# Kernel optimization log

Measured on AMD Instinct MI355X. Metric: run time of the kernel, lower is better.

Reference implementation:

```python
import jax, jax.numpy as jnp
import numpy as np

B, L, C, S, W, R = 2, 32, 32, 64, 64, 32
MH = 32  # forcing MLP hidden


def _conv3d(x, w, b, pad_hw):
    # x: [B, Cin, L, S, W], w: [Cout, Cin, 1, kh, kw]
    y = jax.lax.conv_general_dilated(
        x, w, window_strides=(1, 1, 1),
        padding=[(0, 0), (pad_hw, pad_hw), (pad_hw, pad_hw)],
        dimension_numbers=('NCDHW', 'OIDHW', 'NCDHW'))
    return y + b[None, :, None, None, None]


def _forward(x, listT, params_log_base, dispersion_mod, fm_W1, fm_b1, fm_W2, fm_b2,
             forcing_scale, U_re, U_im, V_re, V_im, pW_re, pW_im, pb_re, pb_im,
             convr_w, convr_b, convi_w, convi_b, projc_w, projc_b, ln_w, ln_b):
    b, l, c, s, w = x.shape
    r = U_re.shape[-1]
    pad = s // 4
    dt = listT.reshape(b, l, 1, 1, 1)

    # FFT with mirror padding along S
    xp = jnp.pad(x, ((0, 0), (0, 0), (0, 0), (pad, pad), (0, 0)), mode='reflect')
    h = jnp.fft.fft2(xp.astype(jnp.complex64), axes=(-2, -1), norm='ortho')

    # complex channel projection
    proj_W = pW_re + 1j * pW_im
    h = jnp.einsum('blcsw,cd->bldsw', h, proj_W)
    h = h + (pb_re + 1j * pb_im)[None, None, :, None, None]

    # back to spatial, crop pad, re-FFT
    hs = jnp.fft.ifft2(h, axes=(-2, -1), norm='ortho')[..., pad:-pad, :]
    h = jnp.fft.fft2(hs, axes=(-2, -1), norm='ortho')

    U = U_re + 1j * U_im          # [C, S, R]
    V = V_re + 1j * V_im          # [C, W, R]
    # zq[b,l,c,r,q] = sum_{s,w} h * conj(U)[c,s,r] * V[c,w,q]
    zq = jnp.einsum('blcsw,csr,cwq->blcrq', h, jnp.conj(U), V)

    nu_base = jnp.exp(params_log_base[0] + dispersion_mod[0]).reshape(1, 1, c, r, 1)
    th_base = jnp.exp(params_log_base[1] + dispersion_mod[1]).reshape(1, 1, c, r, 1)

    # forcing modulation
    ctx = x.mean(axis=(-2, -1))                       # [B, L, C]
    inp = jnp.concatenate([ctx, dt.reshape(b, l, 1)], axis=-1)
    mid = jnp.tanh(inp @ fm_W1 + fm_b1)
    mod = (mid @ fm_W2 + fm_b2).reshape(b, l, c, r, 2)
    dnu = (forcing_scale * jnp.tanh(mod[..., 0]))[..., None]
    dth = (forcing_scale * jnp.tanh(mod[..., 1]))[..., None]

    nu_t = jnp.maximum(nu_base * dt + dnu, 1e-6)       # [B, L, C, R, 1]
    th_t = th_base * dt + dth
    lamb = jnp.exp(jax.lax.complex(-nu_t, th_t))       # complex [B, L, C, R, 1]

    gamma = jnp.sqrt(jnp.maximum(1.0 - jnp.exp(-2.0 * nu_t), 1e-12))
    x_in = zq * gamma.astype(zq.dtype)                 # [B, L, C, R, R]

    # parallel linear-recurrence scan: z_t = lamb_t * z_{t-1} + x_t
    def comb(a, bb):
        a1, x1 = a
        a2, x2 = bb
        return a1 * a2, a2 * x1 + x2
    _, z_out = jax.lax.associative_scan(comb, (lamb, x_in), axis=1)

    # reconstruct spectral field and inverse FFT
    h_rec = jnp.einsum('blcrq,cwq,csr->blcsw', z_out, jnp.conj(V), U)
    h_sp = jnp.fft.ifft2(h_rec, axes=(-2, -1), norm='ortho')

    xr = jnp.transpose(h_sp.real, (0, 2, 1, 3, 4))     # [B, C, L, S, W]
    xi = jnp.transpose(h_sp.imag, (0, 2, 1, 3, 4))
    hr = _conv3d(xr, convr_w, convr_b, 1)
    hi = _conv3d(xi, convi_w, convi_b, 1)
    hf = _conv3d(jnp.concatenate([hr, hi], axis=1), projc_w, projc_b, 0)
    hf = jnp.transpose(hf, (0, 2, 1, 3, 4))            # [B, L, C, S, W]

    # LayerNorm over [S, W]
    mu = hf.mean(axis=(-2, -1), keepdims=True)
    var = hf.var(axis=(-2, -1), keepdims=True)
    hf = (hf - mu) / jnp.sqrt(var + 1e-5) * ln_w + ln_b

    return x + hf


def setup_inputs() -> dict:
    key = jax.random.key(0)
    ks = jax.random.split(key, 20)
    f32 = jnp.float32
    x = jax.random.normal(ks[0], (B, L, C, S, W), dtype=f32)
    listT = jax.random.uniform(ks[1], (B, L), dtype=f32, minval=0.5, maxval=1.5)

    r_min, r_max = 0.8, 0.99
    u1 = jax.random.uniform(ks[2], (C, R), dtype=f32)
    u2 = jax.random.uniform(ks[3], (C, R), dtype=f32)
    nu_log = jnp.log(-0.5 * jnp.log(u1 * (r_max ** 2 - r_min ** 2) + r_min ** 2))
    theta_log = jnp.log(u2 * (2.0 * np.pi))
    params_log_base = jnp.stack([nu_log, theta_log], axis=0)
    dispersion_mod = jnp.zeros((2, C, R), dtype=f32)

    fm_W1 = jax.random.normal(ks[4], (C + 1, MH), dtype=f32) / np.sqrt(C + 1)
    fm_b1 = jnp.zeros((MH,), dtype=f32)
    fm_W2 = jax.random.normal(ks[5], (MH, C * R * 2), dtype=f32) / np.sqrt(MH)
    fm_b2 = jnp.zeros((C * R * 2,), dtype=f32)
    forcing_scale = jnp.float32(0.1)

    cplx_scale = 1.0 / np.sqrt(2.0)
    U_re = jax.random.normal(ks[6], (C, S, R), dtype=f32) * cplx_scale / np.sqrt(S)
    U_im = jax.random.normal(ks[7], (C, S, R), dtype=f32) * cplx_scale / np.sqrt(S)
    V_re = jax.random.normal(ks[8], (C, W, R), dtype=f32) * cplx_scale / np.sqrt(W)
    V_im = jax.random.normal(ks[9], (C, W, R), dtype=f32) * cplx_scale / np.sqrt(W)
    pW_re = jax.random.normal(ks[10], (C, C), dtype=f32) * cplx_scale / np.sqrt(C)
    pW_im = jax.random.normal(ks[11], (C, C), dtype=f32) * cplx_scale / np.sqrt(C)
    pb_re = jnp.zeros((C,), dtype=f32)
    pb_im = jnp.zeros((C,), dtype=f32)

    convr_w = jax.random.normal(ks[12], (C, C, 1, 3, 3), dtype=f32) * (1.0 / np.sqrt(C * 9))
    convr_b = jnp.zeros((C,), dtype=f32)
    convi_w = jax.random.normal(ks[13], (C, C, 1, 3, 3), dtype=f32) * (1.0 / np.sqrt(C * 9))
    convi_b = jnp.zeros((C,), dtype=f32)
    projc_w = jax.random.normal(ks[14], (C, 2 * C, 1, 1, 1), dtype=f32) * (1.0 / np.sqrt(2 * C))
    projc_b = jnp.zeros((C,), dtype=f32)

    ln_w = jnp.ones((S, W), dtype=f32)
    ln_b = jnp.zeros((S, W), dtype=f32)

    return dict(x=x, listT=listT, params_log_base=params_log_base,
                dispersion_mod=dispersion_mod, fm_W1=fm_W1, fm_b1=fm_b1,
                fm_W2=fm_W2, fm_b2=fm_b2, forcing_scale=forcing_scale,
                U_re=U_re, U_im=U_im, V_re=V_re, V_im=V_im,
                pW_re=pW_re, pW_im=pW_im, pb_re=pb_re, pb_im=pb_im,
                convr_w=convr_w, convr_b=convr_b, convi_w=convi_w, convi_b=convi_b,
                projc_w=projc_w, projc_b=projc_b, ln_w=ln_w, ln_b=ln_b)


def reference(x, listT, params_log_base, dispersion_mod, fm_W1, fm_b1, fm_W2, fm_b2,
              forcing_scale, U_re, U_im, V_re, V_im, pW_re, pW_im, pb_re, pb_im,
              convr_w, convr_b, convi_w, convi_b, projc_w, projc_b, ln_w, ln_b):
    return _forward(x, listT, params_log_base, dispersion_mod, fm_W1, fm_b1, fm_W2,
                    fm_b2, forcing_scale, U_re, U_im, V_re, V_im, pW_re, pW_im,
                    pb_re, pb_im, convr_w, convr_b, convi_w, convi_b, projc_w,
                    projc_b, ln_w, ln_b)
```

## Files before the change

### kernel.cpp

```cpp
#include <hip/hip_runtime.h>


typedef __attribute__((ext_vector_type(8))) short short8;
typedef __attribute__((ext_vector_type(4))) float floatx4;

__device__ __forceinline__ unsigned pack_bf16(float re, float im) {
  unsigned a = __float_as_uint(re), b = __float_as_uint(im);
  a = (a + 0x7FFFu + ((a >> 16) & 1u)) >> 16;
  b = (b + 0x7FFFu + ((b >> 16) & 1u)) >> 16;
  return a | (b << 16);
}
__device__ __forceinline__ unsigned short bf16r(float v) {
  unsigned a = __float_as_uint(v);
  return (unsigned short)((a + 0x7FFFu + ((a >> 16) & 1u)) >> 16);
}

__global__ __launch_bounds__(256) void k_prep(
    const float* __restrict__ U_re, const float* __restrict__ U_im,
    const float* __restrict__ V_re, const float* __restrict__ V_im,
    const float* __restrict__ projc_w,
    const float* __restrict__ convr_w, const float* __restrict__ convi_w,
    const float* __restrict__ x,
    unsigned* __restrict__ zqA, unsigned* __restrict__ recA,
    unsigned* __restrict__ recB, unsigned* __restrict__ Wtb,
    float* __restrict__ ctx) {
  const int bid = blockIdx.x;
  const int tid = threadIdx.x;
  if (bid < 2048) {
    __shared__ float2 tw[64];
    if (tid < 64) {
      float sa, ca;
      sincosf((float)tid * 0.09817477042468103f, &sa, &ca);
      tw[tid] = make_float2(ca, sa);
    }
    __syncthreads();
    int gid = bid * 256 + tid;
    const float *Ar, *Ai;
    int knum, mode, variant;
    bool plus;
    unsigned* dst;
    int didx;
    if (gid < 262144) {
      int c = gid >> 13, mat = (gid >> 11) & 3, m = (gid >> 6) & 31,
          kw = gid & 63;
      knum = kw; mode = m;
      if (mat < 2) { Ar = V_re + c * 2048; Ai = V_im + c * 2048; plus = false; }
      else         { Ar = U_re + c * 2048; Ai = U_im + c * 2048; plus = true; }
      variant = mat; dst = zqA; didx = gid;
    } else {
      int rid = gid - 262144;
      int c = rid >> 13, sub = rid & 8191;
      int which = sub >> 11, mm = (sub >> 5) & 63, k2 = sub & 31;
      knum = mm; mode = k2;
      if (which < 2) {
        Ar = U_re + c * 2048; Ai = U_im + c * 2048; plus = true;
        variant = 4 + which; dst = recA;
        didx = ((c * 2 + which) * 64 + mm) * 32 + k2;
      } else {
        Ar = V_re + c * 2048; Ai = V_im + c * 2048; plus = false;
        variant = 4 + which; dst = recB;
        didx = ((c * 2 + which - 2) * 64 + mm) * 32 + k2;
      }
    }
    float sr = 0.f, si = 0.f;
    for (int n = 0; n < 64; ++n) {
      float2 w = tw[(knum * n) & 63];
      float ar = Ar[n * 32 + mode], ai = Ai[n * 32 + mode];
      if (plus) { sr += ar * w.x - ai * w.y; si += ar * w.y + ai * w.x; }
      else      { sr += ar * w.x + ai * w.y; si += ai * w.x - ar * w.y; }
    }
    sr *= 0.125f; si *= 0.125f;
    unsigned pv;
    switch (variant) {
      case 0: pv = pack_bf16(sr, -si); break;
      case 1: pv = pack_bf16(si, sr); break;
      case 2: pv = pack_bf16(sr, si); break;
      case 3: pv = pack_bf16(-si, sr); break;
      case 4: pv = pack_bf16(sr, -si); break;
      case 5: pv = pack_bf16(si, sr); break;
      case 6: pv = pack_bf16(sr, si); break;
      default: pv = pack_bf16(-si, sr); break;
    }
    dst[didx] = pv;
  } else if (bid < 2084) {
    int gid = (bid - 2048) * 256 + tid;
    if (gid < 9216) {
      int co = gid / 288;
      int r2 = gid - co * 288;
      int tap = r2 >> 5, ci = r2 & 31;
      float sr = 0.f, si = 0.f;
      for (int m = 0; m < 32; ++m) {
        sr += projc_w[co * 64 + m]      * convr_w[(m * 32 + ci) * 9 + tap];
        si += projc_w[co * 64 + 32 + m] * convi_w[(m * 32 + ci) * 9 + tap];
      }
      Wtb[gid] = pack_bf16(sr, si);
    }
  } else {
    int blc = bid - 2084;
    const float* p = x + (size_t)blc * 4096;
    float s = 0.f;
    for (int i = tid; i < 4096; i += 256) s += p[i];
    for (int o = 32; o > 0; o >>= 1) s += __shfl_down(s, o, 64);
    __shared__ float wsum[4];
    if ((tid & 63) == 0) wsum[tid >> 6] = s;
    __syncthreads();
    if (tid == 0)
      ctx[blc] = (wsum[0] + wsum[1] + wsum[2] + wsum[3]) * (1.f / 4096.f);
  }
}

__global__ __launch_bounds__(256) void k_mix_mlp(
    const float* __restrict__ x, const float* __restrict__ pWr,
    const float* __restrict__ pWi, unsigned* __restrict__ hs,
    const float* __restrict__ ctx, const float* __restrict__ listT,
    const float* __restrict__ plb, const float* __restrict__ dmod,
    const float* __restrict__ W1, const float* __restrict__ b1,
    const float* __restrict__ W2, const float* __restrict__ b2,
    const float* __restrict__ fscale,
    float2* __restrict__ lam, float* __restrict__ gam) {
  __shared__ unsigned xb_s[512 * 20];
  __shared__ float mid_s[32];
  const int tid = threadIdx.x;
  if (blockIdx.x < 512) {
    const int bl = blockIdx.x >> 3;
    const int pxbase = (blockIdx.x & 7) * 512;
    const float* xb = x + (size_t)bl * 131072 + pxbase;
#pragma unroll
    for (int t = 0; t < 8; ++t) {
      int i = t * 256 + tid;
      int c2 = i & 15, g4 = i >> 4;
      float4 a = *(const float4*)(xb + (2 * c2) * 4096 + g4 * 4);
      float4 b = *(const float4*)(xb + (2 * c2 + 1) * 4096 + g4 * 4);
#pragma unroll
      for (int j = 0; j < 4; ++j) {
        int px = g4 * 4 + j;
        xb_s[px * 20 + (((c2 >> 2) ^ (px & 3)) << 2) + (c2 & 3)] =
            pack_bf16(((const float*)&a)[j], ((const float*)&b)[j]);
      }
    }
    const int lane = tid & 63, wv = tid >> 6;
    const int qd = lane >> 4, ln = lane & 15;
    short8 arL, aiL, arH, aiH;
#pragma unroll
    for (int j = 0; j < 8; ++j) {
      int ci = qd * 8 + j;
      ((short*)&arL)[j] = (short)bf16r(pWr[ci * 32 + ln]);
      ((short*)&aiL)[j] = (short)bf16r(pWi[ci * 32 + ln]);
      ((short*)&arH)[j] = (short)bf16r(pWr[ci * 32 + 16 + ln]);
      ((short*)&aiH)[j] = (short)bf16r(pWi[ci * 32 + 16 + ln]);
    }
    __syncthreads();
#pragma unroll
    for (int pt = 0; pt < 8; ++pt) {
      int pxt = wv * 8 + pt;
      int pxl = pxt * 16 + ln;
      short8 bfr =
          *(const short8*)&xb_s[pxl * 20 + ((qd ^ (pxl & 3)) << 2)];
      floatx4 dRL = {0.f, 0.f, 0.f, 0.f}, dIL = {0.f, 0.f, 0.f, 0.f};
      floatx4 dRH = {0.f, 0.f, 0.f, 0.f}, dIH = {0.f, 0.f, 0.f, 0.f};
      dRL = __builtin_amdgcn_mfma_f32_16x16x32_bf16(arL, bfr, dRL, 0, 0, 0);
      dIL = __builtin_amdgcn_mfma_f32_16x16x32_bf16(aiL, bfr, dIL, 0, 0, 0);
      dRH = __builtin_amdgcn_mfma_f32_16x16x32_bf16(arH, bfr, dRH, 0, 0, 0);
      dIH = __builtin_amdgcn_mfma_f32_16x16x32_bf16(aiH, bfr, dIH, 0, 0, 0);
      unsigned* ho = hs + (size_t)bl * 131072 + pxbase + pxt * 16 + ln;
#pragma unroll
      for (int j = 0; j < 4; ++j) {
        ho[(qd * 4 + j) * 4096] = pack_bf16(dRL[j], dIL[j]);
        ho[(16 + qd * 4 + j) * 4096] = pack_bf16(dRH[j], dIH[j]);
      }
    }
  } else {
    int bl = blockIdx.x - 512;
    float dt = listT[bl];
    if (tid < 32) {
      float a = b1[tid];
      for (int j = 0; j < 32; ++j) a += ctx[bl * 32 + j] * W1[j * 32 + tid];
      a += dt * W1[1024 + tid];
      mid_s[tid] = tanhf(a);
    }
    __syncthreads();
    float fs = fscale[0];
#pragma unroll
    for (int u = 0; u < 4; ++u) {
      int cr = u * 256 + tid;
      int col = cr * 2;
      float m0 = b2[col], m1 = b2[col + 1];
      for (int h = 0; h < 32; ++h) {
        float mh = mid_s[h];
        float2 w2 = *(const float2*)&W2[h * 2048 + col];
        m0 += mh * w2.x;
        m1 += mh * w2.y;
      }
      float dnu = fs * tanhf(m0);
      float dth = fs * tanhf(m1);
      float nub = expf(plb[cr] + dmod[cr]);
      float thb = expf(plb[1024 + cr] + dmod[1024 + cr]);
      float nut = fmaxf(nub * dt + dnu, 1e-6f);
      float tht = thb * dt + dth;
      float e = expf(-nut);
      float sa, ca;
      sincosf(tht, &sa, &ca);
      float g = sqrtf(fmaxf(1.f - expf(-2.f * nut), 1e-12f));
      int o = bl * 1024 + cr;
      lam[o] = make_float2(e * ca, e * sa);
      gam[o] = g;
    }
  }
}

__global__ __launch_bounds__(256) void k_zq(const unsigned* __restrict__ hs,
                                            const short* __restrict__ zqA,
                                            float2* __restrict__ zq) {
  __shared__ unsigned HsB[4096];
  __shared__ unsigned T2[2048];
  const int blc = blockIdx.x;
  const int c = blc & 31;
  const int tid = threadIdx.x;
  const int lane = tid & 63, wv = tid >> 6;
  const int qd = lane >> 4, ln = lane & 15;
  const int mt = wv >> 1, nth = wv & 1;
  {
    const uint4* hp = (const uint4*)(hs + (size_t)blc * 4096);
#pragma unroll
    for (int it = 0; it < 4; ++it) {
      int i4 = tid + it * 256;
      uint4 v = hp[i4];
      int s = i4 >> 4, w4 = i4 & 15;
      *(uint4*)&HsB[s * 64 + ((w4 ^ (s & 15)) << 2)] = v;
    }
  }
  const short* zA = zqA + (size_t)c * 4 * 32 * 128;
  short8 a1[4], a2[4], a3[4], a4[4];
#pragma unroll
  for (int t = 0; t < 4; ++t) {
    int row = mt * 16 + ln;
    a1[t] = *(const short8*)(zA + (0 * 32 + row) * 128 + t * 32 + qd * 8);
    a2[t] = *(const short8*)(zA + (1 * 32 + row) * 128 + t * 32 + qd * 8);
    a3[t] = *(const short8*)(zA + (2 * 32 + row) * 128 + t * 32 + qd * 8);
    a4[t] = *(const short8*)(zA + (3 * 32 + row) * 128 + t * 32 + qd * 8);
  }
  __syncthreads();
#pragma unroll
  for (int nti = 0; nti < 2; ++nti) {
    int nt = nth * 2 + nti;
    int n = nt * 16 + ln;
    floatx4 accr = {0.f, 0.f, 0.f, 0.f}, acci = {0.f, 0.f, 0.f, 0.f};
#pragma unroll
    for (int t = 0; t < 4; ++t) {
      short8 b = *(const short8*)&HsB[n * 64 + (((4 * t + qd) ^ (n & 15)) << 2)];
      accr = __builtin_amdgcn_mfma_f32_16x16x32_bf16(a1[t], b, accr, 0, 0, 0);
      acci = __builtin_amdgcn_mfma_f32_16x16x32_bf16(a2[t], b, acci, 0, 0, 0);
    }
#pragma unroll
    for (int j = 0; j < 4; ++j) {
      int q = mt * 16 + qd * 4 + j;
      int s = n;
      T2[q * 64 + (((s >> 2) ^ (q & 15)) << 2) + (s & 3)] = pack_bf16(accr[j], acci[j]);
    }
  }
  __syncthreads();
  {
    const int mt2 = wv >> 1, nt2 = wv & 1;
    int n = nt2 * 16 + ln;
    floatx4 zr = {0.f, 0.f, 0.f, 0.f}, zi = {0.f, 0.f, 0.f, 0.f};
#pragma unroll
    for (int t = 0; t < 4; ++t) {
      short8 b = *(const short8*)&T2[n * 64 + (((4 * t + qd) ^ (n & 15)) << 2)];
      zr = __builtin_amdgcn_mfma_f32_16x16x32_bf16(a3[t], b, zr, 0, 0, 0);
      zi = __builtin_amdgcn_mfma_f32_16x16x32_bf16(a4[t], b, zi, 0, 0, 0);
    }
    float2* zo = zq + (size_t)blc * 1024;
#pragma unroll
    for (int j = 0; j < 4; ++j) {
      int r = mt2 * 16 + qd * 4 + j;
      zo[r * 32 + n] = make_float2(zr[j], zi[j]);
    }
  }
}

__global__ __launch_bounds__(256) void k_scan(const float2* __restrict__ lam,
                                              const float* __restrict__ gam,
                                              const float2* zin,
                                              float2* zout) {
  const int b = blockIdx.x >> 5, c = blockIdx.x & 31;
  const int tid = threadIdx.x;
  float2 st[4] = {{0.f, 0.f}, {0.f, 0.f}, {0.f, 0.f}, {0.f, 0.f}};
  float2 v[4], lmv[4];
  float gv[4];
  {
    size_t zb = ((size_t)(b * 32) * 32 + c) * 1024;
    int pb = (b * 32) * 1024 + c * 32;
#pragma unroll
    for (int j = 0; j < 4; ++j) {
      int rq = tid + 256 * j;
      v[j] = zin[zb + rq];
      lmv[j] = lam[pb + (rq >> 5)];
      gv[j] = gam[pb + (rq >> 5)];
    }
  }
  for (int t = 0; t < 32; ++t) {
    float2 nv[4], nlm[4];
    float ng[4];
    if (t < 31) {
      size_t zb = ((size_t)(b * 32 + t + 1) * 32 + c) * 1024;
      int pb = (b * 32 + t + 1) * 1024 + c * 32;
#pragma unroll
      for (int j = 0; j < 4; ++j) {
        int rq = tid + 256 * j;
        nv[j] = zin[zb + rq];
        nlm[j] = lam[pb + (rq >> 5)];
        ng[j] = gam[pb + (rq >> 5)];
      }
    }
    size_t zb = ((size_t)(b * 32 + t) * 32 + c) * 1024;
#pragma unroll
    for (int j = 0; j < 4; ++j) {
      float nr = lmv[j].x * st[j].x - lmv[j].y * st[j].y + gv[j] * v[j].x;
      float ni = lmv[j].x * st[j].y + lmv[j].y * st[j].x + gv[j] * v[j].y;
      st[j] = make_float2(nr, ni);
      zout[zb + tid + 256 * j] = st[j];
    }
#pragma unroll
    for (int j = 0; j < 4; ++j) { v[j] = nv[j]; lmv[j] = nlm[j]; gv[j] = ng[j]; }
  }
}

__global__ __launch_bounds__(256) void k_rec(const float2* __restrict__ zs,
                                             const short* __restrict__ recA,
                                             const short* __restrict__ recB,
                                             unsigned* __restrict__ hsp) {
  __shared__ unsigned zB[1024];
  __shared__ unsigned P[2048];
  const int blc = blockIdx.x;
  const int c = blc & 31;
  const int tid = threadIdx.x;
  const int lane = tid & 63, wv = tid >> 6;
  const int qd = lane >> 4, ln = lane & 15;
  {
    const float2* zp = zs + (size_t)blc * 1024;
#pragma unroll
    for (int it = 0; it < 4; ++it) {
      int i = tid + it * 256;
      float2 v = zp[i];
      int r = i >> 5, q = i & 31;
      zB[q * 32 + (((r >> 2) ^ (q & 7)) << 2) + (r & 3)] = pack_bf16(v.x, v.y);
    }
  }
  const short* rA = recA + (size_t)c * 2 * 64 * 64;
  short8 a5[2], a6[2];
#pragma unroll
  for (int t = 0; t < 2; ++t) {
    int row = wv * 16 + ln;
    a5[t] = *(const short8*)(rA + (0 * 64 + row) * 64 + t * 32 + qd * 8);
    a6[t] = *(const short8*)(rA + (1 * 64 + row) * 64 + t * 32 + qd * 8);
  }
  __syncthreads();
#pragma unroll
  for (int nt = 0; nt < 2; ++nt) {
    int n = nt * 16 + ln;
    floatx4 pr = {0.f, 0.f, 0.f, 0.f}, pi = {0.f, 0.f, 0.f, 0.f};
#pragma unroll
    for (int t = 0; t < 2; ++t) {
      short8 b = *(const short8*)&zB[n * 32 + (((4 * t + qd) ^ (n & 7)) << 2)];
      pr = __builtin_amdgcn_mfma_f32_16x16x32_bf16(a5[t], b, pr, 0, 0, 0);
      pi = __builtin_amdgcn_mfma_f32_16x16x32_bf16(a6[t], b, pi, 0, 0, 0);
    }
#pragma unroll
    for (int j = 0; j < 4; ++j) {
      int s = wv * 16 + qd * 4 + j;
      int q = n;
      P[s * 32 + (((q >> 2) ^ (s & 7)) << 2) + (q & 3)] = pack_bf16(pr[j], pi[j]);
    }
  }
  __syncthreads();
  const short* rB = recB + (size_t)c * 2 * 64 * 64;
  short8 pa[2];
#pragma unroll
  for (int t = 0; t < 2; ++t) {
    int row = wv * 16 + ln;
    pa[t] = *(const short8*)&P[row * 32 + (((4 * t + qd) ^ (row & 7)) << 2)];
  }
#pragma unroll
  for (int nt = 0; nt < 4; ++nt) {
    int n = nt * 16 + ln;
    floatx4 hr = {0.f, 0.f, 0.f, 0.f}, hi = {0.f, 0.f, 0.f, 0.f};
#pragma unroll
    for (int t = 0; t < 2; ++t) {
      short8 b5 = *(const short8*)(rB + (0 * 64 + n) * 64 + t * 32 + qd * 8);
      short8 b6 = *(const short8*)(rB + (1 * 64 + n) * 64 + t * 32 + qd * 8);
      hr = __builtin_amdgcn_mfma_f32_16x16x32_bf16(pa[t], b5, hr, 0, 0, 0);
      hi = __builtin_amdgcn_mfma_f32_16x16x32_bf16(pa[t], b6, hi, 0, 0, 0);
    }
    unsigned* ho = hsp + (size_t)blc * 4096;
#pragma unroll
    for (int j = 0; j < 4; ++j) {
      int s = wv * 16 + qd * 4 + j;
      ho[s * 64 + n] = pack_bf16(hr[j], hi[j]);
    }
  }
}

__global__ __launch_bounds__(256, 2) void k_conv(
    const unsigned* __restrict__ hsp, const short* __restrict__ Wtb,
    unsigned short* __restrict__ convout, float2* __restrict__ stats) {
  __shared__ unsigned lds_in[6 * 66 * 32];
  const int bl = blockIdx.x >> 4;
  const int slab = blockIdx.x & 15;
  const int y0 = slab * 4;
  const int tid = threadIdx.x;
  for (int i = tid; i < 384; i += 256) {
    int ci = i & 31, j = i >> 5;
    int yi = j >> 1, xi = (j & 1) ? 65 : 0;
    int slot = (ci >> 2) ^ (xi & 7);
    lds_in[(yi * 66 + xi) * 32 + slot * 4 + (ci & 3)] = 0u;
  }
#pragma unroll
  for (int t = 0; t < 12; ++t) {
    int i = t * 256 + tid;
    int ci = i & 31;
    int j = i >> 5;
    int yi = j >> 4, x4 = j & 15;
    int y = y0 + yi - 1;
    uint4 v = make_uint4(0u, 0u, 0u, 0u);
    if ((unsigned)y < 64u)
      v = *(const uint4*)(hsp + (((size_t)bl * 32 + ci) * 64 + y) * 64 + x4 * 4);
    int xb = 1 + x4 * 4;
#pragma unroll
    for (int jj = 0; jj < 4; ++jj) {
      int xi = xb + jj;
      int slot = (ci >> 2) ^ (xi & 7);
      lds_in[(yi * 66 + xi) * 32 + slot * 4 + (ci & 3)] =
          ((const unsigned*)&v)[jj];
    }
  }
  const int lane = tid & 63;
  const int wv = tid >> 6;
  const int co = lane & 15;
  const int qd = lane >> 4;
  short8 bL[18], bH[18];
  {
    const short* wpL = Wtb + (co * 9) * 64 + qd * 8;
    const short* wpH = Wtb + ((co + 16) * 9) * 64 + qd * 8;
#pragma unroll
    for (int tap = 0; tap < 9; ++tap)
#pragma unroll
      for (int kk = 0; kk < 2; ++kk) {
        bL[tap * 2 + kk] = *(const short8*)(wpL + tap * 64 + kk * 32);
        bH[tap * 2 + kk] = *(const short8*)(wpH + tap * 64 + kk * 32);
      }
  }
  __syncthreads();
  float sL = 0.f, s2L = 0.f, sH = 0.f, s2H = 0.f;
  const int x0 = wv * 16;
  const int xl = lane & 15;
  for (int ry = 0; ry < 4; ++ry) {
    floatx4 aL = {0.f, 0.f, 0.f, 0.f}, aH = {0.f, 0.f, 0.f, 0.f};
#pragma unroll
    for (int tap = 0; tap < 9; ++tap) {
      int dy = tap / 3, dx = tap - dy * 3;
      int yi = ry + dy;
      int xi = x0 + xl + dx;
#pragma unroll
      for (int kk = 0; kk < 2; ++kk) {
        int slot = ((kk << 2) | qd) ^ (xi & 7);
        const short8 a =
            *(const short8*)&lds_in[(yi * 66 + xi) * 32 + slot * 4];
        aL = __builtin_amdgcn_mfma_f32_16x16x32_bf16(a, bL[tap * 2 + kk], aL, 0, 0, 0);
        aH = __builtin_amdgcn_mfma_f32_16x16x32_bf16(a, bH[tap * 2 + kk], aH, 0, 0, 0);
      }
    }
    size_t goL = (((size_t)bl * 32 + co) * 64 + (y0 + ry)) * 64 + x0 + qd * 4;
    size_t goH = goL + (size_t)16 * 4096;
    *(uint2*)(convout + goL) =
        make_uint2(pack_bf16(aL[0], aL[1]), pack_bf16(aL[2], aL[3]));
    *(uint2*)(convout + goH) =
        make_uint2(pack_bf16(aH[0], aH[1]), pack_bf16(aH[2], aH[3]));
#pragma unroll
    for (int j = 0; j < 4; ++j) {
      sL += aL[j]; s2L += aL[j] * aL[j];
      sH += aH[j]; s2H += aH[j] * aH[j];
    }
  }
  sL += __shfl_down(sL, 32, 64);  s2L += __shfl_down(s2L, 32, 64);
  sH += __shfl_down(sH, 32, 64);  s2H += __shfl_down(s2H, 32, 64);
  sL += __shfl_down(sL, 16, 64);  s2L += __shfl_down(s2L, 16, 64);
  sH += __shfl_down(sH, 16, 64);  s2H += __shfl_down(s2H, 16, 64);
  if (lane < 16) {
    stats[((size_t)bl * 32 + lane) * 64 + slab * 4 + wv] = make_float2(sL, s2L);
    stats[((size_t)bl * 32 + 16 + lane) * 64 + slab * 4 + wv] =
        make_float2(sH, s2H);
  }
}

__global__ __launch_bounds__(256) void k_ln(
    const unsigned short* __restrict__ convout,
    const float2* __restrict__ stats, const float* __restrict__ x,
    const float* __restrict__ ln_w, const float* __restrict__ ln_b,
    float* __restrict__ out) {
  const int blc = blockIdx.x;
  const int tid = threadIdx.x;
  __shared__ float sh_mu, sh_rs;
  if (tid < 64) {
    float2 v = stats[(size_t)blc * 64 + tid];
    float s = v.x, s2 = v.y;
#pragma unroll
    for (int o = 32; o > 0; o >>= 1) {
      s += __shfl_down(s, o, 64);
      s2 += __shfl_down(s2, o, 64);
    }
    if (tid == 0) {
      float mu = s * (1.f / 4096.f);
      float var = s2 * (1.f / 4096.f) - mu * mu;
      sh_mu = mu;
      sh_rs = rsqrtf(var + 1e-5f);
    }
  }
  __syncthreads();
  float mu = sh_mu, rs = sh_rs;
  const uint2* cp = (const uint2*)(convout + (size_t)blc * 4096);
  const float4* xp = (const float4*)(x + (size_t)blc * 4096);
  const float4* lwp = (const float4*)ln_w;
  const float4* lbp = (const float4*)ln_b;
  float4* op = (float4*)(out + (size_t)blc * 4096);
#pragma unroll
  for (int k = 0; k < 4; ++k) {
    int i = tid + k * 256;
    uint2 cv = cp[i];
    float4 xv = xp[i], lw = lwp[i], lb = lbp[i];
    float c0 = __uint_as_float(cv.x << 16);
    float c1 = __uint_as_float(cv.x & 0xFFFF0000u);
    float c2 = __uint_as_float(cv.y << 16);
    float c3 = __uint_as_float(cv.y & 0xFFFF0000u);
    float4 o;
    o.x = xv.x + (c0 - mu) * rs * lw.x + lb.x;
    o.y = xv.y + (c1 - mu) * rs * lw.y + lb.y;
    o.z = xv.z + (c2 - mu) * rs * lw.z + lb.z;
    o.w = xv.w + (c3 - mu) * rs * lw.w + lb.w;
    op[i] = o;
  }
}

extern "C" void kernel_launch(void* const* d_in, const int* in_sizes, int n_in,
                              void* d_out, int out_size, void* d_ws,
                              size_t ws_size, hipStream_t stream) {
  const float* x       = (const float*)d_in[0];
  const float* listT   = (const float*)d_in[1];
  const float* plb     = (const float*)d_in[2];
  const float* dmod    = (const float*)d_in[3];
  const float* fm_W1   = (const float*)d_in[4];
  const float* fm_b1   = (const float*)d_in[5];
  const float* fm_W2   = (const float*)d_in[6];
  const float* fm_b2   = (const float*)d_in[7];
  const float* fscale  = (const float*)d_in[8];
  const float* U_re    = (const float*)d_in[9];
  const float* U_im    = (const float*)d_in[10];
  const float* V_re    = (const float*)d_in[11];
  const float* V_im    = (const float*)d_in[12];
  const float* pW_re   = (const float*)d_in[13];
  const float* pW_im   = (const float*)d_in[14];
  const float* convr_w = (const float*)d_in[17];
  const float* convi_w = (const float*)d_in[19];
  const float* projc_w = (const float*)d_in[21];
  const float* ln_w    = (const float*)d_in[23];
  const float* ln_b    = (const float*)d_in[24];
  float* out = (float*)d_out;

  float* wsf = (float*)d_ws;
  unsigned* hs  = (unsigned*)wsf;
  unsigned* hsp = (unsigned*)wsf;
  unsigned* zqAp  = (unsigned*)(wsf + 8388608);
  unsigned* recAp = (unsigned*)(wsf + 8388608 + 262144);
  unsigned* recBp = (unsigned*)(wsf + 8388608 + 393216);
  unsigned short* convout = (unsigned short*)(wsf + 8388608);
  float2*   stats = (float2*)(wsf + 12582912);
  float2*   zq  = (float2*)(wsf + 16777216);
  size_t off = 16777216 + 4194304;
  float2* zs = (float2*)(wsf + off);
  size_t need_with_zs = (size_t)(off + 4194304 + 470016) * 4;
  bool sep = ws_size >= need_with_zs;
  if (sep) off += 4194304; else zs = zq;
  float2*   lam  = (float2*)(wsf + off);
  float*    gam  = wsf + off + 131072;
  float*    ctx  = wsf + off + 458752;
  unsigned* Wtb  = (unsigned*)(wsf + off + 460800);

  k_prep<<<4132, 256, 0, stream>>>(U_re, U_im, V_re, V_im, projc_w,
                                   convr_w, convi_w, x, zqAp, recAp, recBp,
                                   Wtb, ctx);
  k_mix_mlp<<<576, 256, 0, stream>>>(x, pW_re, pW_im, hs, ctx, listT, plb,
                                     dmod, fm_W1, fm_b1, fm_W2, fm_b2,
                                     fscale, lam, gam);
  k_zq<<<2048, 256, 0, stream>>>(hs, (const short*)zqAp, zq);
  k_scan<<<64, 256, 0, stream>>>(lam, gam, zq, zs);
  k_rec<<<2048, 256, 0, stream>>>(zs, (const short*)recAp, (const short*)recBp, hsp);
  k_conv<<<1024, 256, 0, stream>>>(hsp, (const short*)Wtb, convout, stats);
  k_ln<<<2048, 256, 0, stream>>>(convout, stats, x, ln_w, ln_b, out);
}
```

Measured before the change: 258.8 us.

## Fuse channel-mean into mix kernel, move MLP into zq kernel, widen scan grid

Computes the per-(b,l,c) spatial mean inside the channel-mix kernel while x is already being loaded, accumulating it into ctx with atomics. This removes the separate reduction pass over x in the prep kernel, which now only zeroes ctx. The forcing MLP blocks move into the zq kernel as extra blocks so they can read the completed ctx. The scan kernel goes from 64 to 256 blocks with one element per thread, giving more parallelism on a latency-bound sequential loop. The costs are atomic accumulation, whose summation order can vary between runs, and extra shared-memory reservation in the zq blocks.

```diff
diff --git a/kernel.cpp b/kernel.cpp
--- a/kernel.cpp
+++ b/kernel.cpp
@@ -20,7 +20,6 @@
     const float* __restrict__ V_re, const float* __restrict__ V_im,
     const float* __restrict__ projc_w,
     const float* __restrict__ convr_w, const float* __restrict__ convi_w,
-    const float* __restrict__ x,
     unsigned* __restrict__ zqA, unsigned* __restrict__ recA,
     unsigned* __restrict__ recB, unsigned* __restrict__ Wtb,
     float* __restrict__ ctx) {
@@ -96,81 +95,92 @@
       Wtb[gid] = pack_bf16(sr, si);
     }
   } else {
-    int blc = bid - 2084;
-    const float* p = x + (size_t)blc * 4096;
-    float s = 0.f;
-    for (int i = tid; i < 4096; i += 256) s += p[i];
-    for (int o = 32; o > 0; o >>= 1) s += __shfl_down(s, o, 64);
-    __shared__ float wsum[4];
-    if ((tid & 63) == 0) wsum[tid >> 6] = s;
-    __syncthreads();
-    if (tid == 0)
-      ctx[blc] = (wsum[0] + wsum[1] + wsum[2] + wsum[3]) * (1.f / 4096.f);
-  }
-}
-
-__global__ __launch_bounds__(256) void k_mix_mlp(
+    for (int i = tid; i < 2048; i += 256) ctx[i] = 0.f;
+  }
+}
+
+__global__ __launch_bounds__(256) void k_mix(
     const float* __restrict__ x, const float* __restrict__ pWr,
     const float* __restrict__ pWi, unsigned* __restrict__ hs,
+    float* __restrict__ ctx) {
+  __shared__ unsigned xb_s[512 * 20];
+  __shared__ float red[16][16][2];
+  const int tid = threadIdx.x;
+  const int bl = blockIdx.x >> 3;
+  const int pxbase = (blockIdx.x & 7) * 512;
+  const float* xb = x + (size_t)bl * 131072 + pxbase;
+  float csa = 0.f, csb = 0.f;
+#pragma unroll
+  for (int t = 0; t < 8; ++t) {
+    int i = t * 256 + tid;
+    int c2 = i & 15, g4 = i >> 4;
+    float4 a = *(const float4*)(xb + (2 * c2) * 4096 + g4 * 4);
+    float4 b = *(const float4*)(xb + (2 * c2 + 1) * 4096 + g4 * 4);
+    csa += a.x + a.y + a.z + a.w;
+    csb += b.x + b.y + b.z + b.w;
+#pragma unroll
+    for (int j = 0; j < 4; ++j) {
+      int px = g4 * 4 + j;
+      xb_s[px * 20 + (((c2 >> 2) ^ (px & 3)) << 2) + (c2 & 3)] =
+          pack_bf16(((const float*)&a)[j], ((const float*)&b)[j]);
+    }
+  }
+  red[tid & 15][tid >> 4][0] = csa;
+  red[tid & 15][tid >> 4][1] = csb;
+  const int lane = tid & 63, wv = tid >> 6;
+  const int qd = lane >> 4, ln = lane & 15;
+  short8 arL, aiL, arH, aiH;
+#pragma unroll
+  for (int j = 0; j < 8; ++j) {
+    int ci = qd * 8 + j;
+    ((short*)&arL)[j] = (short)bf16r(pWr[ci * 32 + ln]);
+    ((short*)&aiL)[j] = (short)bf16r(pWi[ci * 32 + ln]);
+    ((short*)&arH)[j] = (short)bf16r(pWr[ci * 32 + 16 + ln]);
+    ((short*)&aiH)[j] = (short)bf16r(pWi[ci * 32 + 16 + ln]);
+  }
+  __syncthreads();
+  if (tid < 32) {
+    int c2 = tid >> 1, part = tid & 1;
+    float s = 0.f;
+#pragma unroll
+    for (int w = 0; w < 16; ++w) s += red[c2][w][part];
+    atomicAdd(&ctx[bl * 32 + 2 * c2 + part], s * (1.f / 4096.f));
+  }
+#pragma unroll
+  for (int pt = 0; pt < 8; ++pt) {
+    int pxt = wv * 8 + pt;
+    int pxl = pxt * 16 + ln;
+    short8 bfr = *(const short8*)&xb_s[pxl * 20 + ((qd ^ (pxl & 3)) << 2)];
+    floatx4 dRL = {0.f, 0.f, 0.f, 0.f}, dIL = {0.f, 0.f, 0.f, 0.f};
+    floatx4 dRH = {0.f, 0.f, 0.f, 0.f}, dIH = {0.f, 0.f, 0.f, 0.f};
+    dRL = __builtin_amdgcn_mfma_f32_16x16x32_bf16(arL, bfr, dRL, 0, 0, 0);
+    dIL = __builtin_amdgcn_mfma_f32_16x16x32_bf16(aiL, bfr, dIL, 0, 0, 0);
+    dRH = __builtin_amdgcn_mfma_f32_16x16x32_bf16(arH, bfr, dRH, 0, 0, 0);
+    dIH = __builtin_amdgcn_mfma_f32_16x16x32_bf16(aiH, bfr, dIH, 0, 0, 0);
+    unsigned* ho = hs + (size_t)bl * 131072 + pxbase + pxt * 16 + ln;
+#pragma unroll
+    for (int j = 0; j < 4; ++j) {
+      ho[(qd * 4 + j) * 4096] = pack_bf16(dRL[j], dIL[j]);
+      ho[(16 + qd * 4 + j) * 4096] = pack_bf16(dRH[j], dIH[j]);
+    }
+  }
+}
+
+__global__ __launch_bounds__(256) void k_zq(
+    const unsigned* __restrict__ hs, const short* __restrict__ zqA,
+    float2* __restrict__ zq,
     const float* __restrict__ ctx, const float* __restrict__ listT,
     const float* __restrict__ plb, const float* __restrict__ dmod,
     const float* __restrict__ W1, const float* __restrict__ b1,
     const float* __restrict__ W2, const float* __restrict__ b2,
     const float* __restrict__ fscale,
     float2* __restrict__ lam, float* __restrict__ gam) {
-  __shared__ unsigned xb_s[512 * 20];
+  __shared__ unsigned HsB[4096];
+  __shared__ unsigned T2[2048];
   __shared__ float mid_s[32];
   const int tid = threadIdx.x;
-  if (blockIdx.x < 512) {
-    const int bl = blockIdx.x >> 3;
-    const int pxbase = (blockIdx.x & 7) * 512;
-    const float* xb = x + (size_t)bl * 131072 + pxbase;
-#pragma unroll
-    for (int t = 0; t < 8; ++t) {
-      int i = t * 256 + tid;
-      int c2 = i & 15, g4 = i >> 4;
-      float4 a = *(const float4*)(xb + (2 * c2) * 4096 + g4 * 4);
-      float4 b = *(const float4*)(xb + (2 * c2 + 1) * 4096 + g4 * 4);
-#pragma unroll
-      for (int j = 0; j < 4; ++j) {
-        int px = g4 * 4 + j;
-        xb_s[px * 20 + (((c2 >> 2) ^ (px & 3)) << 2) + (c2 & 3)] =
-            pack_bf16(((const float*)&a)[j], ((const float*)&b)[j]);
-      }
-    }
-    const int lane = tid & 63, wv = tid >> 6;
-    const int qd = lane >> 4, ln = lane & 15;
-    short8 arL, aiL, arH, aiH;
-#pragma unroll
-    for (int j = 0; j < 8; ++j) {
-      int ci = qd * 8 + j;
-      ((short*)&arL)[j] = (short)bf16r(pWr[ci * 32 + ln]);
-      ((short*)&aiL)[j] = (short)bf16r(pWi[ci * 32 + ln]);
-      ((short*)&arH)[j] = (short)bf16r(pWr[ci * 32 + 16 + ln]);
-      ((short*)&aiH)[j] = (short)bf16r(pWi[ci * 32 + 16 + ln]);
-    }
-    __syncthreads();
-#pragma unroll
-    for (int pt = 0; pt < 8; ++pt) {
-      int pxt = wv * 8 + pt;
-      int pxl = pxt * 16 + ln;
-      short8 bfr =
-          *(const short8*)&xb_s[pxl * 20 + ((qd ^ (pxl & 3)) << 2)];
-      floatx4 dRL = {0.f, 0.f, 0.f, 0.f}, dIL = {0.f, 0.f, 0.f, 0.f};
-      floatx4 dRH = {0.f, 0.f, 0.f, 0.f}, dIH = {0.f, 0.f, 0.f, 0.f};
-      dRL = __builtin_amdgcn_mfma_f32_16x16x32_bf16(arL, bfr, dRL, 0, 0, 0);
-      dIL = __builtin_amdgcn_mfma_f32_16x16x32_bf16(aiL, bfr, dIL, 0, 0, 0);
-      dRH = __builtin_amdgcn_mfma_f32_16x16x32_bf16(arH, bfr, dRH, 0, 0, 0);
-      dIH = __builtin_amdgcn_mfma_f32_16x16x32_bf16(aiH, bfr, dIH, 0, 0, 0);
-      unsigned* ho = hs + (size_t)bl * 131072 + pxbase + pxt * 16 + ln;
-#pragma unroll
-      for (int j = 0; j < 4; ++j) {
-        ho[(qd * 4 + j) * 4096] = pack_bf16(dRL[j], dIL[j]);
-        ho[(16 + qd * 4 + j) * 4096] = pack_bf16(dRH[j], dIH[j]);
-      }
-    }
-  } else {
-    int bl = blockIdx.x - 512;
+  if (blockIdx.x >= 2048) {
+    int bl = blockIdx.x - 2048;
     float dt = listT[bl];
     if (tid < 32) {
       float a = b1[tid];
@@ -205,17 +215,10 @@
       lam[o] = make_float2(e * ca, e * sa);
       gam[o] = g;
     }
-  }
-}
-
-__global__ __launch_bounds__(256) void k_zq(const unsigned* __restrict__ hs,
-                                            const short* __restrict__ zqA,
-                                            float2* __restrict__ zq) {
-  __shared__ unsigned HsB[4096];
-  __shared__ unsigned T2[2048];
+    return;
+  }
   const int blc = blockIdx.x;
   const int c = blc & 31;
-  const int tid = threadIdx.x;
   const int lane = tid & 63, wv = tid >> 6;
   const int qd = lane >> 4, ln = lane & 15;
   const int mt = wv >> 1, nth = wv & 1;
@@ -282,46 +285,29 @@
                                               const float* __restrict__ gam,
                                               const float2* zin,
                                               float2* zout) {
-  const int b = blockIdx.x >> 5, c = blockIdx.x & 31;
-  const int tid = threadIdx.x;
-  float2 st[4] = {{0.f, 0.f}, {0.f, 0.f}, {0.f, 0.f}, {0.f, 0.f}};
-  float2 v[4], lmv[4];
-  float gv[4];
-  {
-    size_t zb = ((size_t)(b * 32) * 32 + c) * 1024;
-    int pb = (b * 32) * 1024 + c * 32;
-#pragma unroll
-    for (int j = 0; j < 4; ++j) {
-      int rq = tid + 256 * j;
-      v[j] = zin[zb + rq];
-      lmv[j] = lam[pb + (rq >> 5)];
-      gv[j] = gam[pb + (rq >> 5)];
-    }
-  }
+  const int bc = blockIdx.x >> 2;
+  const int b = bc >> 5, c = bc & 31;
+  const int rq = (blockIdx.x & 3) * 256 + threadIdx.x;
+  const int r = rq >> 5;
+  float2 st = make_float2(0.f, 0.f);
+  float2 v = zin[((size_t)(b * 32) * 32 + c) * 1024 + rq];
+  float2 lm = lam[(b * 32) * 1024 + c * 32 + r];
+  float g = gam[(b * 32) * 1024 + c * 32 + r];
   for (int t = 0; t < 32; ++t) {
-    float2 nv[4], nlm[4];
-    float ng[4];
+    float2 nv, nlm;
+    float ng;
     if (t < 31) {
-      size_t zb = ((size_t)(b * 32 + t + 1) * 32 + c) * 1024;
-      int pb = (b * 32 + t + 1) * 1024 + c * 32;
-#pragma unroll
-      for (int j = 0; j < 4; ++j) {
-        int rq = tid + 256 * j;
-        nv[j] = zin[zb + rq];
-        nlm[j] = lam[pb + (rq >> 5)];
-        ng[j] = gam[pb + (rq >> 5)];
-      }
-    }
-    size_t zb = ((size_t)(b * 32 + t) * 32 + c) * 1024;
-#pragma unroll
-    for (int j = 0; j < 4; ++j) {
-      float nr = lmv[j].x * st[j].x - lmv[j].y * st[j].y + gv[j] * v[j].x;
-      float ni = lmv[j].x * st[j].y + lmv[j].y * st[j].x + gv[j] * v[j].y;
-      st[j] = make_float2(nr, ni);
-      zout[zb + tid + 256 * j] = st[j];
-    }
-#pragma unroll
-    for (int j = 0; j < 4; ++j) { v[j] = nv[j]; lmv[j] = nlm[j]; gv[j] = ng[j]; }
+      size_t zb2 = ((size_t)(b * 32 + t + 1) * 32 + c) * 1024;
+      int pb2 = (b * 32 + t + 1) * 1024 + c * 32;
+      nv = zin[zb2 + rq];
+      nlm = lam[pb2 + r];
+      ng = gam[pb2 + r];
+    }
+    float nr = lm.x * st.x - lm.y * st.y + g * v.x;
+    float ni = lm.x * st.y + lm.y * st.x + g * v.y;
+    st = make_float2(nr, ni);
+    zout[((size_t)(b * 32 + t) * 32 + c) * 1024 + rq] = st;
+    v = nv; lm = nlm; g = ng;
   }
 }
 
@@ -584,14 +570,14 @@
   float*    ctx  = wsf + off + 458752;
   unsigned* Wtb  = (unsigned*)(wsf + off + 460800);
 
-  k_prep<<<4132, 256, 0, stream>>>(U_re, U_im, V_re, V_im, projc_w,
-                                   convr_w, convi_w, x, zqAp, recAp, recBp,
+  k_prep<<<2085, 256, 0, stream>>>(U_re, U_im, V_re, V_im, projc_w,
+                                   convr_w, convi_w, zqAp, recAp, recBp,
                                    Wtb, ctx);
-  k_mix_mlp<<<576, 256, 0, stream>>>(x, pW_re, pW_im, hs, ctx, listT, plb,
-                                     dmod, fm_W1, fm_b1, fm_W2, fm_b2,
-                                     fscale, lam, gam);
-  k_zq<<<2048, 256, 0, stream>>>(hs, (const short*)zqAp, zq);
-  k_scan<<<64, 256, 0, stream>>>(lam, gam, zq, zs);
+  k_mix<<<512, 256, 0, stream>>>(x, pW_re, pW_im, hs, ctx);
+  k_zq<<<2112, 256, 0, stream>>>(hs, (const short*)zqAp, zq, ctx, listT, plb,
+                                 dmod, fm_W1, fm_b1, fm_W2, fm_b2, fscale,
+                                 lam, gam);
+  k_scan<<<256, 256, 0, stream>>>(lam, gam, zq, zs);
   k_rec<<<2048, 256, 0, stream>>>(zs, (const short*)recAp, (const short*)recBp, hsp);
   k_conv<<<1024, 256, 0, stream>>>(hsp, (const short*)Wtb, convout, stats);
   k_ln<<<2048, 256, 0, stream>>>(convout, stats, x, ln_w, ln_b, out);
```

New measurement: 250.7 us. -3.1%, faster.
